# Performance work log

Hardware: AMD Instinct MI355X
Metric: run time of the kernel (lower is better)

## Reference

```python
import jax, jax.numpy as jnp
import numpy as np
from jax import lax

B, C, H, W = 64, 3, 256, 256
E, D = 64, 32          # expert_nums, embed_dim
TOP_K = 2
NOISE_EPS = 0.01
ALPHA = 0.8


def setup_inputs() -> dict:
    key = jax.random.key(0)
    ks = jax.random.split(key, 16)
    n = lambda k, shape, s=0.05: jax.random.normal(k, shape, jnp.float32) * s
    return {
        "task_id": jax.random.randint(ks[0], (B,), 0, 10),
        "degradation_info": jax.random.normal(ks[1], (B, C, H, W), jnp.float32),
        "noise": jax.random.normal(ks[2], (B, E), jnp.float32),
        "mlp_w1": n(ks[3], (1, D)), "mlp_b1": jnp.zeros((D,), jnp.float32),
        "mlp_w2": n(ks[4], (D, D)), "mlp_b2": jnp.zeros((D,), jnp.float32),
        "conv1_w": n(ks[5], (16, C, 3, 3)), "conv1_b": jnp.zeros((16,), jnp.float32),
        "conv2_w": n(ks[6], (32, 16, 3, 3)), "conv2_b": jnp.zeros((32,), jnp.float32),
        "deg_w": n(ks[7], (32, D)), "deg_b": jnp.zeros((D,), jnp.float32),
        "expert_keys": jax.random.normal(ks[8], (E, D), jnp.float32),
        "gate_w": n(ks[9], (E, E)), "gate_b": jnp.zeros((E,), jnp.float32),
        "noise_w": n(ks[10], (E, E)), "noise_b": jnp.zeros((E,), jnp.float32),
    }


def _conv(x, w):
    return lax.conv_general_dilated(
        x, w, window_strides=(1, 1), padding="SAME",
        dimension_numbers=("NCHW", "OIHW", "NCHW"))


def reference(task_id, degradation_info, noise,
              mlp_w1, mlp_b1, mlp_w2, mlp_b2,
              conv1_w, conv1_b, conv2_w, conv2_b,
              deg_w, deg_b, expert_keys,
              gate_w, gate_b, noise_w, noise_b):
    # task embedding: Linear(1,D) -> ReLU -> Linear(D,D)
    t = task_id.astype(jnp.float32)[:, None]                       # [B,1]
    task_embed = jax.nn.relu(t @ mlp_w1 + mlp_b1) @ mlp_w2 + mlp_b2  # [B,D]

    # degradation conv embed: conv->relu->conv->relu->global avg pool
    h = jax.nn.relu(_conv(degradation_info, conv1_w) + conv1_b[None, :, None, None])
    h = jax.nn.relu(_conv(h, conv2_w) + conv2_b[None, :, None, None])
    feat = h.mean(axis=(2, 3))                                     # [B,32]
    deg_embed = feat @ deg_w + deg_b                               # [B,D]

    combined = task_embed + (1.0 - ALPHA) * deg_embed              # [B,D]
    sim = combined @ expert_keys.T / jnp.sqrt(jnp.float32(D))      # [B,E]
    expert_weight = jax.nn.softmax(sim, axis=1)

    clean_logits = expert_weight @ gate_w + gate_b                 # [B,E]
    stddev = jax.nn.softplus(expert_weight @ noise_w + noise_b) + NOISE_EPS
    logits = clean_logits + noise * stddev                         # train=True path

    top_logits, top_idx = lax.top_k(logits, min(TOP_K + 1, E))
    tk_logits = top_logits[:, :TOP_K]                              # [B,k]
    tk_idx = top_idx[:, :TOP_K]
    tk_gates = jax.nn.softmax(tk_logits, axis=1)

    rows = jnp.arange(logits.shape[0])[:, None]
    gates = jnp.zeros_like(logits).at[rows, tk_idx].set(tk_gates)  # scatter
    load = gates.sum(axis=0)                                       # [E]
    return gates, load
```

## Files before the change

kernel.cpp:

```cpp
#include <hip/hip_runtime.h>
#include <math.h>

typedef __attribute__((ext_vector_type(8)))  short  short8;
typedef __attribute__((ext_vector_type(4)))  short  svec4;
typedef __attribute__((ext_vector_type(4)))  float  floatx4;
typedef __attribute__((ext_vector_type(16))) float  floatx16;
typedef __attribute__((ext_vector_type(2)))  float  floatx2;
typedef __attribute__((ext_vector_type(2)))  unsigned uintx2;

__device__ __forceinline__ short bf16rne(float f) {
    unsigned u = __float_as_uint(f);
    unsigned r = (u + 0x7FFFu + ((u >> 16) & 1u)) >> 16;
    return (short)r;
}
__device__ __forceinline__ unsigned pk2(float a, float b) {
#if __has_builtin(__builtin_amdgcn_cvt_pk_bf16_f32)
    auto t = __builtin_amdgcn_cvt_pk_bf16_f32(a, b);
    unsigned u; __builtin_memcpy(&u, &t, 4); return u;
#else
    return (unsigned)(unsigned short)bf16rne(a) |
           ((unsigned)(unsigned short)bf16rne(b) << 16);
#endif
}

#define WS_FRAG_OFF  8192
#define WS_BIAS1_OFF (WS_FRAG_OFF + 11 * 64 * 16)
#define WS_BIAS2_OFF (WS_BIAS1_OFF + 64 * 16)

#define PLANE_B 18496

__global__ __launch_bounds__(256) void build_frags_kernel(
    const float* __restrict__ w1,
    const float* __restrict__ b1,
    const float* __restrict__ w2,
    const float* __restrict__ b2,
    void* __restrict__ ws,
    float* __restrict__ out)
{
    const int t = threadIdx.x;
    float* feat = (float*)ws;
    for (int i = t; i < 2048; i += 256) feat[i] = 0.0f;
    if (t >= 64 && t < 128) out[4096 + (t - 64)] = 0.0f;

    if (t < 64) {
        const int lane = t;
        const int q = lane >> 4, ml = lane & 15;
        const int n32 = lane & 31, half = lane >> 5;
        short8* F = (short8*)((char*)ws + WS_FRAG_OFF);

        short8 W1a;
#pragma unroll
        for (int j = 0; j < 8; ++j) {
            int p = q * 2 + (j >> 2), c = j & 3;
            W1a[j] = (c < 3) ? bf16rne(w1[ml * 27 + c * 9 + p]) : (short)0;
        }
        F[0 * 64 + lane] = W1a;

        short8 W1b;
#pragma unroll
        for (int j = 0; j < 8; ++j) {
            W1b[j] = (q == 0 && j < 3) ? bf16rne(w1[ml * 27 + j * 9 + 8])
                                       : (short)0;
        }
        F[1 * 64 + lane] = W1b;

#pragma unroll
        for (int s = 0; s < 9; ++s) {
            short8 Bs;
#pragma unroll
            for (int j = 0; j < 8; ++j) {
                int ic = half * 8 + j;
                Bs[j] = bf16rne(w2[(n32 * 16 + ic) * 9 + s]);
            }
            F[(2 + s) * 64 + lane] = Bs;
        }
        floatx4 bv;
#pragma unroll
        for (int r = 0; r < 4; ++r) bv[r] = b1[q * 4 + r];
        ((floatx4*)((char*)ws + WS_BIAS1_OFF))[lane] = bv;
        ((float*)((char*)ws + WS_BIAS2_OFF))[lane] = b2[n32];
    }
}

__device__ __forceinline__ void conv1_tile(
    char* __restrict__ wptr, const char* __restrict__ inb,
    const int* lcB, int gbyte, int wbyte, bool valid, bool wmask,
    short8 W1a, short8 W1b, floatx4 biasv)
{
    svec4 r0 = *(const svec4*)(inb + gbyte + lcB[0]);
    svec4 r1 = *(const svec4*)(inb + gbyte + lcB[1]);
    svec4 r2 = *(const svec4*)(inb + gbyte + lcB[2]);
    short8 Bx, By;
    Bx[0]=r0[0]; Bx[1]=r0[1]; Bx[2]=r0[2]; Bx[3]=r0[3];
    Bx[4]=r1[0]; Bx[5]=r1[1]; Bx[6]=r1[2]; Bx[7]=r1[3];
    By[0]=r2[0]; By[1]=r2[1]; By[2]=r2[2]; By[3]=r2[3];
    By[4]=r2[0]; By[5]=r2[1]; By[6]=r2[2]; By[7]=r2[3];
    floatx4 acc = __builtin_amdgcn_mfma_f32_16x16x32_bf16(W1a, Bx, biasv,
                                                          0, 0, 0);
    acc = __builtin_amdgcn_mfma_f32_16x16x32_bf16(W1b, By, acc, 0, 0, 0);
    float v0 = fmaxf(acc[0], 0.f), v1 = fmaxf(acc[1], 0.f);
    float v2 = fmaxf(acc[2], 0.f), v3 = fmaxf(acc[3], 0.f);
    if (!valid) { v0 = 0.f; v1 = 0.f; v2 = 0.f; v3 = 0.f; }
    if (wmask) {
        uintx2 w; w.x = pk2(v0, v1); w.y = pk2(v2, v3);
        *(uintx2*)(wptr + wbyte) = w;
    }
}

__global__ __launch_bounds__(256, 3) void conv_feat_kernel(
    const float* __restrict__ x,
    const void*  __restrict__ ws_ro,
    float* __restrict__ feat_sum)
{
    __shared__ short s_in4[36 * 36 * 4];
    __shared__ short s_h1[2 * 9248];
    __shared__ float s_part[4][32];

    const int t    = threadIdx.x;
    const int lane = t & 63, wv = t >> 6;
    const int q    = lane >> 4, ml = lane & 15;
    const int n32  = lane & 31, half = lane >> 5;
    const int tx = blockIdx.x, ty = blockIdx.y, b = blockIdx.z;
    const bool border = (tx == 0) | (tx == 7) | (ty == 0) | (ty == 7);

    const short8* F = (const short8*)((const char*)ws_ro + WS_FRAG_OFF);
    short8 W1a = F[0 * 64 + lane];
    short8 W1b = F[1 * 64 + lane];
    short8 B2[9];
#pragma unroll
    for (int s = 0; s < 9; ++s) B2[s] = F[(2 + s) * 64 + lane];
    floatx4 biasv = ((const floatx4*)((const char*)ws_ro + WS_BIAS1_OFF))[lane];
    float   b2v   = ((const float*)((const char*)ws_ro + WS_BIAS2_OFF))[lane];

    int lcB[3];
    {
        int p0 = q * 2, p1 = q * 2 + 1;
        lcB[0] = ((p0 / 3) * 36 + p0 % 3) * 8;
        lcB[1] = ((p1 / 3) * 36 + p1 % 3) * 8;
        lcB[2] = (2 * 36 + 2) * 8;
    }

    const int gy0 = ty * 32 - 2, gx0 = tx * 32 - 2;
    const float* xb = x + (size_t)b * 3 * 65536;
    {
        int r = t / 36, c = t - (t / 36) * 36;
        short* sp = &s_in4[t * 4];
        if (!border) {
            const float* p = xb + (gy0 + r) * 256 + gx0 + c;
            for (int i = t; i < 1296; i += 256) {
                float v0 = p[0], v1 = p[65536], v2 = p[131072];
                uintx2 w; w.x = pk2(v0, v1); w.y = pk2(v2, 0.f);
                *(uintx2*)sp = w;
                c += 4;
                int bump = (c >= 36);
                c -= bump ? 36 : 0;
                p += 7 * 256 + 4 + (bump ? 256 : 0);
                sp += 1024;
            }
        } else {
            for (int i = t; i < 1296; i += 256) {
                int gy = gy0 + r, gx = gx0 + c;
                float v0 = 0.f, v1 = 0.f, v2 = 0.f;
                if ((unsigned)gy < 256u && (unsigned)gx < 256u) {
                    const float* p = xb + gy * 256 + gx;
                    v0 = p[0]; v1 = p[65536]; v2 = p[131072];
                }
                uintx2 w; w.x = pk2(v0, v1); w.y = pk2(v2, 0.f);
                *(uintx2*)sp = w;
                c += 4; r += 7;
                if (c >= 36) { c -= 36; r += 1; }
                sp += 1024;
            }
        }
    }
    __syncthreads();

    char* wptr = (char*)s_h1 + (q >> 1) * PLANE_B + (q & 1) * 8;
    const char* inb = (const char*)s_in4;
    const int mlb = ml * 8, ml16 = ml * 16;
    if (!border) {
#pragma unroll
        for (int i = 0; i < 17; ++i) {
            int u = wv * 17 + i, row = u >> 1, ch = u & 1;
            conv1_tile(wptr, inb, lcB, row * 288 + ch * 128 + mlb,
                       row * 544 + ch * 256 + ml16, true, true,
                       W1a, W1b, biasv);
        }
        {
            int col = 32 + (wv >> 1), rb = (wv & 1) * 16;
            conv1_tile(wptr, inb, lcB, (rb + ml) * 288 + col * 8,
                       ml * 544 + (rb * 34 + col) * 16, true, true,
                       W1a, W1b, biasv);
        }
        if (wv == 0) {
            int ml2 = ml & 3;
            int iy = 32 + (ml2 >> 1), ix = 32 + (ml2 & 1);
            conv1_tile(wptr, inb, lcB, iy * 288 + ix * 8,
                       (iy * 34 + ix) * 16, true, ml < 4, W1a, W1b, biasv);
        }
    } else {
        const bool gxOK0 = (unsigned)(tx * 32 - 1 + ml) < 256u;
        const bool gxOK1 = (unsigned)(tx * 32 + 15 + ml) < 256u;
#pragma unroll
        for (int i = 0; i < 17; ++i) {
            int u = wv * 17 + i, row = u >> 1, ch = u & 1;
            bool ok = ((unsigned)(ty * 32 - 1 + row) < 256u) &
                      (ch ? gxOK1 : gxOK0);
            conv1_tile(wptr, inb, lcB, row * 288 + ch * 128 + mlb,
                       row * 544 + ch * 256 + ml16, ok, true,
                       W1a, W1b, biasv);
        }
        {
            int col = 32 + (wv >> 1), rb = (wv & 1) * 16;
            bool ok = ((unsigned)(ty * 32 - 1 + rb + ml) < 256u) &
                      ((unsigned)(tx * 32 - 1 + col) < 256u);
            conv1_tile(wptr, inb, lcB, (rb + ml) * 288 + col * 8,
                       ml * 544 + (rb * 34 + col) * 16, ok, true,
                       W1a, W1b, biasv);
        }
        if (wv == 0) {
            int ml2 = ml & 3;
            int iy = 32 + (ml2 >> 1), ix = 32 + (ml2 & 1);
            bool ok = ((unsigned)(ty * 32 - 1 + iy) < 256u) &
                      ((unsigned)(tx * 32 - 1 + ix) < 256u);
            conv1_tile(wptr, inb, lcB, iy * 288 + ix * 8,
                       (iy * 34 + ix) * 16, ok, ml < 4, W1a, W1b, biasv);
        }
    }
    __syncthreads();

    float part;
    {
        const int prow0 = n32 >> 4, pcol = n32 & 15;
        const int ch = wv >> 1, tp0 = (wv & 1) * 8;
        const int ox = ch * 16 + pcol;
        const char* pl = (const char*)s_h1 + half * PLANE_B;
        int pb = ((2 * tp0 + prow0) * 34 + ox) * 16;
        short8 Af[3][3];
#pragma unroll
        for (int ky = 0; ky < 3; ++ky)
#pragma unroll
            for (int kx = 0; kx < 3; ++kx)
                Af[ky][kx] = *(const short8*)(pl + pb + (ky * 34 + kx) * 16);

        floatx16 bias16;
#pragma unroll
        for (int r = 0; r < 16; ++r) bias16[r] = b2v;

        floatx2 p2 = {0.f, 0.f};
#pragma unroll
        for (int it = 0; it < 8; ++it) {
            const int rb = (2 * it) % 3;
            __builtin_amdgcn_s_setprio(1);
            floatx16 acc = __builtin_amdgcn_mfma_f32_32x32x16_bf16(
                    Af[rb][0], B2[0], bias16, 0, 0, 0);
#pragma unroll
            for (int s = 1; s < 9; ++s) {
                const int ky = s / 3, kx = s % 3;
                acc = __builtin_amdgcn_mfma_f32_32x32x16_bf16(
                        Af[(rb + ky) % 3][kx], B2[s], acc, 0, 0, 0);
            }
            __builtin_amdgcn_s_setprio(0);
#pragma unroll
            for (int r = 0; r < 16; r += 2) {
                floatx2 t2 = {fmaxf(acc[r], 0.0f), fmaxf(acc[r + 1], 0.0f)};
                p2 += t2;
            }
            if (it < 7) {
                pb += 1088;
#pragma unroll
                for (int kx = 0; kx < 3; ++kx) {
                    Af[rb][kx] =
                        *(const short8*)(pl + pb + (1 * 34 + kx) * 16);
                    Af[(rb + 1) % 3][kx] =
                        *(const short8*)(pl + pb + (2 * 34 + kx) * 16);
                }
            }
        }
        part = p2.x + p2.y;
    }
    part += __shfl_xor(part, 32);
    if (lane < 32) s_part[wv][n32] = part;
    __syncthreads();
    if (t < 32) {
        float ssum = s_part[0][t] + s_part[1][t] + s_part[2][t] + s_part[3][t];
        atomicAdd(feat_sum + b * 32 + t, ssum);
    }
}

__global__ __launch_bounds__(64) void router_gate_kernel(
    const int* __restrict__ task_id,
    const float* __restrict__ noise,
    const float* __restrict__ mlp_w1,
    const float* __restrict__ mlp_b1,
    const float* __restrict__ mlp_w2,
    const float* __restrict__ mlp_b2,
    const float* __restrict__ deg_w,
    const float* __restrict__ deg_b,
    const float* __restrict__ keys,
    const float* __restrict__ gate_w,
    const float* __restrict__ gate_b,
    const float* __restrict__ noise_w,
    const float* __restrict__ noise_b,
    const float* __restrict__ feat_sum,
    float* __restrict__ out)
{
    const int b = blockIdx.x;
    const int e = threadIdx.x;

    __shared__ float s_te[32];
    __shared__ float s_comb[32];
    __shared__ float s_ew[64];

    if (e < 32) {
        float tf = (float)task_id[b];
        s_te[e] = fmaxf(tf * mlp_w1[e] + mlp_b1[e], 0.0f);
    }
    __syncthreads();
    if (e < 32) {
        float acc = mlp_b2[e];
        for (int k = 0; k < 32; ++k) acc += s_te[k] * mlp_w2[k * 32 + e];
        float dacc = deg_b[e];
        for (int c = 0; c < 32; ++c)
            dacc += (feat_sum[b * 32 + c] * (1.0f / 65536.0f)) * deg_w[c * 32 + e];
        s_comb[e] = acc + 0.2f * dacc;
    }
    __syncthreads();

    float s = 0.0f;
    for (int d = 0; d < 32; ++d) s += s_comb[d] * keys[e * 32 + d];
    s *= 0.17677669529663687f;

    float m = s;
    for (int off = 32; off; off >>= 1) m = fmaxf(m, __shfl_xor(m, off));
    float p = expf(s - m);
    float sum = p;
    for (int off = 32; off; off >>= 1) sum += __shfl_xor(sum, off);
    float w = p / sum;
    s_ew[e] = w;
    __syncthreads();

    float cl = gate_b[e], nz = noise_b[e];
    for (int k = 0; k < 64; ++k) {
        float ewk = s_ew[k];
        cl += ewk * gate_w[k * 64 + e];
        nz += ewk * noise_w[k * 64 + e];
    }
    float sp = (nz > 20.0f) ? nz : log1pf(expf(nz));
    float logit = cl + noise[b * 64 + e] * (sp + 0.01f);

    float v0 = logit; int i0 = e;
    for (int off = 32; off; off >>= 1) {
        float ov = __shfl_xor(v0, off);
        int   oi = __shfl_xor(i0, off);
        if (ov > v0 || (ov == v0 && oi < i0)) { v0 = ov; i0 = oi; }
    }
    float v1 = (e == i0) ? -INFINITY : logit; int i1 = e;
    for (int off = 32; off; off >>= 1) {
        float ov = __shfl_xor(v1, off);
        int   oi = __shfl_xor(i1, off);
        if (ov > v1 || (ov == v1 && oi < i1)) { v1 = ov; i1 = oi; }
    }

    float e1 = expf(v1 - v0);
    float g0 = 1.0f / (1.0f + e1);
    float g1 = e1 / (1.0f + e1);

    float g = (e == i0) ? g0 : (e == i1) ? g1 : 0.0f;
    out[b * 64 + e] = g;
    if (g != 0.0f) atomicAdd(out + 64 * 64 + e, g);
}

extern "C" void kernel_launch(void* const* d_in, const int* in_sizes, int n_in,
                              void* d_out, int out_size, void* d_ws, size_t ws_size,
                              hipStream_t stream) {
    const int*   task_id = (const int*)d_in[0];
    const float* x       = (const float*)d_in[1];
    const float* noise   = (const float*)d_in[2];
    const float* mlp_w1  = (const float*)d_in[3];
    const float* mlp_b1  = (const float*)d_in[4];
    const float* mlp_w2  = (const float*)d_in[5];
    const float* mlp_b2  = (const float*)d_in[6];
    const float* conv1_w = (const float*)d_in[7];
    const float* conv1_b = (const float*)d_in[8];
    const float* conv2_w = (const float*)d_in[9];
    const float* conv2_b = (const float*)d_in[10];
    const float* deg_w   = (const float*)d_in[11];
    const float* deg_b   = (const float*)d_in[12];
    const float* keys    = (const float*)d_in[13];
    const float* gate_w  = (const float*)d_in[14];
    const float* gate_b  = (const float*)d_in[15];
    const float* noise_w = (const float*)d_in[16];
    const float* noise_b = (const float*)d_in[17];

    float* out  = (float*)d_out;
    float* feat = (float*)d_ws;

    build_frags_kernel<<<1, 256, 0, stream>>>(conv1_w, conv1_b, conv2_w,
                                              conv2_b, d_ws, out);
    dim3 gridA(8, 8, 64);
    conv_feat_kernel<<<gridA, 256, 0, stream>>>(x, d_ws, feat);
    router_gate_kernel<<<64, 64, 0, stream>>>(
        task_id, noise, mlp_w1, mlp_b1, mlp_w2, mlp_b2, deg_w, deg_b, keys,
        gate_w, gate_b, noise_w, noise_b, feat, out);
}
```

Measured before the change: 177.1 us.

## Use packed max/shuffles, simplify input staging loop, drop setprio around MFMA

Replaces scalar fmaxf ReLU with a packed elementwise max on float2 pairs, builds MFMA B operands with shufflevector instead of per-element assignment, and rewrites the input staging loop to recompute row/column by division rather than incremental pointer bumps. It also removes the s_setprio raising around the conv2 MFMA chain. These are several small instruction-level tweaks meant to cut VALU work and scheduling overhead, at the risk of adding integer division cost and changing wave scheduling priority.

```diff
diff --git a/kernel.cpp b/kernel.cpp
--- a/kernel.cpp
+++ b/kernel.cpp
@@ -20,6 +20,14 @@
 #else
     return (unsigned)(unsigned short)bf16rne(a) |
            ((unsigned)(unsigned short)bf16rne(b) << 16);
+#endif
+}
+__device__ __forceinline__ floatx2 pkmax0(floatx2 a) {
+#if __has_builtin(__builtin_elementwise_max)
+    floatx2 z = {0.f, 0.f};
+    return __builtin_elementwise_max(a, z);
+#else
+    floatx2 r; r.x = fmaxf(a.x, 0.f); r.y = fmaxf(a.y, 0.f); return r;
 #endif
 }
 
@@ -90,19 +98,16 @@
     svec4 r0 = *(const svec4*)(inb + gbyte + lcB[0]);
     svec4 r1 = *(const svec4*)(inb + gbyte + lcB[1]);
     svec4 r2 = *(const svec4*)(inb + gbyte + lcB[2]);
-    short8 Bx, By;
-    Bx[0]=r0[0]; Bx[1]=r0[1]; Bx[2]=r0[2]; Bx[3]=r0[3];
-    Bx[4]=r1[0]; Bx[5]=r1[1]; Bx[6]=r1[2]; Bx[7]=r1[3];
-    By[0]=r2[0]; By[1]=r2[1]; By[2]=r2[2]; By[3]=r2[3];
-    By[4]=r2[0]; By[5]=r2[1]; By[6]=r2[2]; By[7]=r2[3];
+    short8 Bx = __builtin_shufflevector(r0, r1, 0, 1, 2, 3, 4, 5, 6, 7);
+    short8 By = __builtin_shufflevector(r2, r0, 0, 1, 2, 3, 4, 5, 6, 7);
     floatx4 acc = __builtin_amdgcn_mfma_f32_16x16x32_bf16(W1a, Bx, biasv,
                                                           0, 0, 0);
     acc = __builtin_amdgcn_mfma_f32_16x16x32_bf16(W1b, By, acc, 0, 0, 0);
-    float v0 = fmaxf(acc[0], 0.f), v1 = fmaxf(acc[1], 0.f);
-    float v2 = fmaxf(acc[2], 0.f), v3 = fmaxf(acc[3], 0.f);
-    if (!valid) { v0 = 0.f; v1 = 0.f; v2 = 0.f; v3 = 0.f; }
+    floatx2 lo = {acc[0], acc[1]}, hi = {acc[2], acc[3]};
+    lo = pkmax0(lo); hi = pkmax0(hi);
+    if (!valid) { floatx2 z = {0.f, 0.f}; lo = z; hi = z; }
     if (wmask) {
-        uintx2 w; w.x = pk2(v0, v1); w.y = pk2(v2, v3);
+        uintx2 w; w.x = pk2(lo.x, lo.y); w.y = pk2(hi.x, hi.y);
         *(uintx2*)(wptr + wbyte) = w;
     }
 }
@@ -142,35 +147,25 @@
 
     const int gy0 = ty * 32 - 2, gx0 = tx * 32 - 2;
     const float* xb = x + (size_t)b * 3 * 65536;
-    {
-        int r = t / 36, c = t - (t / 36) * 36;
-        short* sp = &s_in4[t * 4];
-        if (!border) {
+    if (!border) {
+        for (int i = t; i < 1296; i += 256) {
+            int r = i / 36, c = i - r * 36;
             const float* p = xb + (gy0 + r) * 256 + gx0 + c;
-            for (int i = t; i < 1296; i += 256) {
-                float v0 = p[0], v1 = p[65536], v2 = p[131072];
-                uintx2 w; w.x = pk2(v0, v1); w.y = pk2(v2, 0.f);
-                *(uintx2*)sp = w;
-                c += 4;
-                int bump = (c >= 36);
-                c -= bump ? 36 : 0;
-                p += 7 * 256 + 4 + (bump ? 256 : 0);
-                sp += 1024;
-            }
-        } else {
-            for (int i = t; i < 1296; i += 256) {
-                int gy = gy0 + r, gx = gx0 + c;
-                float v0 = 0.f, v1 = 0.f, v2 = 0.f;
-                if ((unsigned)gy < 256u && (unsigned)gx < 256u) {
-                    const float* p = xb + gy * 256 + gx;
-                    v0 = p[0]; v1 = p[65536]; v2 = p[131072];
-                }
-                uintx2 w; w.x = pk2(v0, v1); w.y = pk2(v2, 0.f);
-                *(uintx2*)sp = w;
-                c += 4; r += 7;
-                if (c >= 36) { c -= 36; r += 1; }
-                sp += 1024;
-            }
+            float v0 = p[0], v1 = p[65536], v2 = p[131072];
+            uintx2 w; w.x = pk2(v0, v1); w.y = pk2(v2, 0.f);
+            *(uintx2*)&s_in4[i * 4] = w;
+        }
+    } else {
+        for (int i = t; i < 1296; i += 256) {
+            int r = i / 36, c = i - r * 36;
+            int gy = gy0 + r, gx = gx0 + c;
+            float v0 = 0.f, v1 = 0.f, v2 = 0.f;
+            if ((unsigned)gy < 256u && (unsigned)gx < 256u) {
+                const float* p = xb + gy * 256 + gx;
+                v0 = p[0]; v1 = p[65536]; v2 = p[131072];
+            }
+            uintx2 w; w.x = pk2(v0, v1); w.y = pk2(v2, 0.f);
+            *(uintx2*)&s_in4[i * 4] = w;
         }
     }
     __syncthreads();
@@ -251,7 +246,6 @@
 #pragma unroll
         for (int it = 0; it < 8; ++it) {
             const int rb = (2 * it) % 3;
-            __builtin_amdgcn_s_setprio(1);
             floatx16 acc = __builtin_amdgcn_mfma_f32_32x32x16_bf16(
                     Af[rb][0], B2[0], bias16, 0, 0, 0);
 #pragma unroll
@@ -260,11 +254,10 @@
                 acc = __builtin_amdgcn_mfma_f32_32x32x16_bf16(
                         Af[(rb + ky) % 3][kx], B2[s], acc, 0, 0, 0);
             }
-            __builtin_amdgcn_s_setprio(0);
 #pragma unroll
             for (int r = 0; r < 16; r += 2) {
-                floatx2 t2 = {fmaxf(acc[r], 0.0f), fmaxf(acc[r + 1], 0.0f)};
-                p2 += t2;
+                floatx2 a2 = {acc[r], acc[r + 1]};
+                p2 += pkmax0(a2);
             }
             if (it < 7) {
                 pb += 1088;
```

Result: no change. 176.4 us (-0.4%).
